# Kernel optimization log

Measured on AMD Instinct MI355X. Metric: run time of the kernel, lower is better.

## Reference

```python
import jax, jax.numpy as jnp
import numpy as np

C_M, C_Z, H, C = 256, 128, 8, 32  # msa emb, pair emb, heads, head channels
S, R = 128, 256                   # MSA rows, residues


def layer_norm(x, gamma, beta, eps=1e-5):
    mu = jnp.mean(x, axis=-1, keepdims=True)
    var = jnp.var(x, axis=-1, keepdims=True)
    return (x - mu) * jax.lax.rsqrt(var + eps) * gamma + beta


def setup_inputs() -> dict:
    key = jax.random.key(0)
    ks = jax.random.split(key, 12)
    sc_m = 1.0 / np.sqrt(C_M)
    sc_z = 1.0 / np.sqrt(C_Z)
    sc_hc = 1.0 / np.sqrt(H * C)
    return {
        "msa_rep": jax.random.normal(ks[0], (S, R, C_M), dtype=jnp.float32),
        "pair_rep": jax.random.normal(ks[1], (R, R, C_Z), dtype=jnp.float32),
        "ln_msa_g": jnp.ones((C_M,), jnp.float32),
        "ln_msa_b": jnp.zeros((C_M,), jnp.float32),
        "ln_pair_g": jnp.ones((C_Z,), jnp.float32),
        "ln_pair_b": jnp.zeros((C_Z,), jnp.float32),
        "w_q": jax.random.normal(ks[2], (C_M, H, C), jnp.float32) * sc_m,
        "w_k": jax.random.normal(ks[3], (C_M, H, C), jnp.float32) * sc_m,
        "w_v": jax.random.normal(ks[4], (C_M, H, C), jnp.float32) * sc_m,
        "w_g": jax.random.normal(ks[5], (C_M, H, C), jnp.float32) * sc_m,
        "b_g": jnp.zeros((H, C), jnp.float32),
        "w_b": jax.random.normal(ks[6], (C_Z, H), jnp.float32) * sc_z,
        "b_b": jnp.zeros((H,), jnp.float32),
        "w_o": jax.random.normal(ks[7], (H, C, C_M), jnp.float32) * sc_hc,
        "b_o": jnp.zeros((C_M,), jnp.float32),
    }


def reference(msa_rep, pair_rep, ln_msa_g, ln_msa_b, ln_pair_g, ln_pair_b,
              w_q, w_k, w_v, w_g, b_g, w_b, b_b, w_o, b_o):
    m = layer_norm(msa_rep, ln_msa_g, ln_msa_b)                 # [S,R,C_M]
    q = jnp.einsum('src,chd->srhd', m, w_q)                     # [S,R,H,C]
    k = jnp.einsum('src,chd->srhd', m, w_k)
    v = jnp.einsum('src,chd->srhd', m, w_v)
    gates = jax.nn.sigmoid(jnp.einsum('src,chd->srhd', m, w_g) + b_g)
    # pair bias: [R,R,H] -> [H,R,R]
    z = layer_norm(pair_rep, ln_pair_g, ln_pair_b)
    b = jnp.einsum('ijc,ch->hij', z, w_b) + b_b[:, None, None]  # [H,R,R]
    logits = jnp.einsum('sqhd,skhd->shqk', q, k) / np.sqrt(C)   # [S,H,R,R]
    logits = logits + b[None]
    w = jax.nn.softmax(logits, axis=-1)
    o = jnp.einsum('shqk,skhd->sqhd', w, v)                     # [S,R,H,C]
    o = gates * o
    out = jnp.einsum('srhd,hdc->src', o, w_o) + b_o             # [S,R,C_M]
    return out
```

## Files before the change

kernel.cpp:

```cpp
#include <hip/hip_runtime.h>
#include <hip/hip_bf16.h>

#define S_DIM 128
#define R_DIM 256
#define CM 256
#define CZ 128
#define H_DIM 8
#define C_DIM 32

typedef short bf16x8 __attribute__((ext_vector_type(8)));
typedef float f32x4 __attribute__((ext_vector_type(4)));

__device__ inline ushort f2b(float f) {
  __hip_bfloat16 b = __float2bfloat16(f);
  return *(ushort*)&b;
}
__device__ inline float b2f(ushort u) {
  __hip_bfloat16 b = *(__hip_bfloat16*)&u;
  return __bfloat162float(b);
}

__device__ __forceinline__ void gld_lds16(const ushort* g, ushort* l) {
  __builtin_amdgcn_global_load_lds(
      (const __attribute__((address_space(1))) unsigned int*)g,
      (__attribute__((address_space(3))) unsigned int*)l, 16, 0, 0);
}

__global__ __launch_bounds__(256) void wt_kernel(
    const float* __restrict__ wq, const float* __restrict__ wk,
    const float* __restrict__ wv, const float* __restrict__ wg,
    const float* __restrict__ wo, ushort* __restrict__ Wt5) {
  __shared__ float t[64][65];
  int z = blockIdx.z;
  const float* W = (z == 0) ? wq : (z == 1) ? wk : (z == 2) ? wv
                   : (z == 3) ? wg : wo;
  ushort* Wt = Wt5 + (size_t)z * 65536;
  int tid = threadIdx.x;
  int r = tid >> 2, c4 = (tid & 3) * 16;
  int rowBase = blockIdx.y * 64, colBase = blockIdx.x * 64;
#pragma unroll
  for (int j = 0; j < 16; ++j)
    t[r][c4 + j] = W[(size_t)(rowBase + r) * 256 + colBase + c4 + j];
  __syncthreads();
#pragma unroll
  for (int j = 0; j < 16; ++j)
    Wt[(size_t)(colBase + r) * 256 + rowBase + c4 + j] = f2b(t[c4 + j][r]);
}

__global__ __launch_bounds__(256) void ln_msa_kernel(
    const float* __restrict__ x, const float* __restrict__ g,
    const float* __restrict__ b, ushort* __restrict__ m) {
  int lane = threadIdx.x & 63, w = threadIdx.x >> 6;
  int row = blockIdx.x * 4 + w;
  const float* xp = x + (size_t)row * CM + lane * 4;
  float4 v = *(const float4*)xp;
  float s1 = v.x + v.y + v.z + v.w;
  float s2 = v.x * v.x + v.y * v.y + v.z * v.z + v.w * v.w;
#pragma unroll
  for (int off = 32; off; off >>= 1) {
    s1 += __shfl_xor(s1, off, 64);
    s2 += __shfl_xor(s2, off, 64);
  }
  float mean = s1 * (1.0f / CM);
  float rstd = rsqrtf(s2 * (1.0f / CM) - mean * mean + 1e-5f);
  float4 gv = *(const float4*)(g + lane * 4);
  float4 bv = *(const float4*)(b + lane * 4);
  ushort4 o;
  o.x = f2b((v.x - mean) * rstd * gv.x + bv.x);
  o.y = f2b((v.y - mean) * rstd * gv.y + bv.y);
  o.z = f2b((v.z - mean) * rstd * gv.z + bv.z);
  o.w = f2b((v.w - mean) * rstd * gv.w + bv.w);
  *(ushort4*)(m + (size_t)row * CM + lane * 4) = o;
}

__global__ __launch_bounds__(256) void pair_bias_kernel(
    const float* __restrict__ z, const float* __restrict__ g,
    const float* __restrict__ b, const float* __restrict__ w_b,
    const float* __restrict__ b_b, float* __restrict__ bias) {
  __shared__ float wbs[CZ][8];
  __shared__ float gs[CZ], bs[CZ];
  int tid = threadIdx.x;
  if (tid < CZ) { gs[tid] = g[tid]; bs[tid] = b[tid]; }
  for (int i = tid; i < CZ * 8; i += 256) wbs[i >> 3][i & 7] = w_b[i];
  __syncthreads();
  int q = tid & 3;
  int row = blockIdx.x * 64 + (tid >> 2);
  const float* zp = z + (size_t)row * CZ + q * 32;
  float4 v[8];
#pragma unroll
  for (int j = 0; j < 8; ++j) v[j] = *(const float4*)(zp + j * 4);
  float s1 = 0.f, s2 = 0.f;
#pragma unroll
  for (int j = 0; j < 8; ++j) {
    s1 += v[j].x + v[j].y + v[j].z + v[j].w;
    s2 += v[j].x * v[j].x + v[j].y * v[j].y + v[j].z * v[j].z +
          v[j].w * v[j].w;
  }
  s1 += __shfl_xor(s1, 1, 64);
  s2 += __shfl_xor(s2, 1, 64);
  s1 += __shfl_xor(s1, 2, 64);
  s2 += __shfl_xor(s2, 2, 64);
  float mean = s1 * (1.0f / CZ);
  float var = s2 * (1.0f / CZ) - mean * mean;
  float rstd = rsqrtf(var + 1e-5f);
  float acc[8] = {};
#pragma unroll
  for (int j = 0; j < 8; ++j) {
    float e[4] = {v[j].x, v[j].y, v[j].z, v[j].w};
#pragma unroll
    for (int u = 0; u < 4; ++u) {
      int c = q * 32 + j * 4 + u;
      float zn = (e[u] - mean) * rstd * gs[c] + bs[c];
#pragma unroll
      for (int h = 0; h < 8; ++h) acc[h] += zn * wbs[c][h];
    }
  }
#pragma unroll
  for (int h = 0; h < 8; ++h) {
    acc[h] += __shfl_xor(acc[h], 1, 64);
    acc[h] += __shfl_xor(acc[h], 2, 64);
  }
  int h0 = q * 2;
  bias[(size_t)h0 * (R_DIM * R_DIM) + row] = acc[h0] + b_b[h0];
  bias[(size_t)(h0 + 1) * (R_DIM * R_DIM) + row] = acc[h0 + 1] + b_b[h0 + 1];
}

__global__ __launch_bounds__(256) void proj_mfma(
    const ushort* __restrict__ M, const ushort* __restrict__ Wt5,
    const float* __restrict__ b_g, ushort* __restrict__ qb,
    ushort* __restrict__ kb2, ushort* __restrict__ vb,
    ushort* __restrict__ gb) {
  __shared__ ushort As[128 * 64];
  __shared__ ushort Bs[64 * 64];
  int tid = threadIdx.x, lane = tid & 63, wid = tid >> 6;
  int lr = lane & 15, lg = lane >> 4;
  int rowBase = blockIdx.x * 128;
  int cby = blockIdx.y;
  int proj = cby >> 2;
  int sc = (lane & 7) ^ ((lane >> 3) & 7);
  const ushort* Ag =
      M + (size_t)(rowBase + wid * 32 + (lane >> 3)) * 256 + sc * 8;
  const ushort* Bg =
      Wt5 + (size_t)(cby * 64 + wid * 16 + (lane >> 3)) * 256 + sc * 8;
  ushort* Asl = As + wid * (32 * 64);
  ushort* Bsl = Bs + wid * (16 * 64);
  int wr = wid >> 1, wc = wid & 1;
  int sx = (lr & 7) * 8;
  f32x4 zf = {0.f, 0.f, 0.f, 0.f};
  f32x4 acc[4][2];
#pragma unroll
  for (int i = 0; i < 4; ++i)
#pragma unroll
    for (int j = 0; j < 2; ++j) acc[i][j] = zf;

  for (int kb = 0; kb < 4; ++kb) {
    if (kb) __syncthreads();
#pragma unroll
    for (int c = 0; c < 4; ++c)
      gld_lds16(Ag + kb * 64 + c * (8 * 256), Asl + c * (8 * 64));
#pragma unroll
    for (int c = 0; c < 2; ++c)
      gld_lds16(Bg + kb * 64 + c * (8 * 256), Bsl + c * (8 * 64));
    __syncthreads();
#pragma unroll
    for (int kk = 0; kk < 2; ++kk) {
      bf16x8 a[4], b[2];
#pragma unroll
      for (int mf = 0; mf < 4; ++mf)
        a[mf] = *(const bf16x8*)&As[(wr * 64 + mf * 16 + lr) * 64 +
                                    ((kk * 32 + lg * 8) ^ sx)];
#pragma unroll
      for (int nf = 0; nf < 2; ++nf)
        b[nf] = *(const bf16x8*)&Bs[(wc * 32 + nf * 16 + lr) * 64 +
                                    ((kk * 32 + lg * 8) ^ sx)];
#pragma unroll
      for (int mf = 0; mf < 4; ++mf)
#pragma unroll
        for (int nf = 0; nf < 2; ++nf)
          acc[mf][nf] = __builtin_amdgcn_mfma_f32_16x16x32_bf16(
              b[nf], a[mf], acc[mf][nf], 0, 0, 0);
    }
  }
#pragma unroll
  for (int mf = 0; mf < 4; ++mf) {
    int row = rowBase + wr * 64 + mf * 16 + lr;
    int s = row >> 8, rr = row & 255;
#pragma unroll
    for (int nf = 0; nf < 2; ++nf) {
      int colL = (cby & 3) * 64 + wc * 32 + nf * 16 + lg * 4;
      int h = colL >> 5, d0 = colL & 31;
      size_t oidx = ((size_t)((s * H_DIM + h) * R_DIM + rr)) * C_DIM + d0;
      f32x4 v4 = acc[mf][nf];
      ushort4 o4;
      if (proj == 0) {
        o4.x = f2b(v4[0] * 0.17677669529663687f);
        o4.y = f2b(v4[1] * 0.17677669529663687f);
        o4.z = f2b(v4[2] * 0.17677669529663687f);
        o4.w = f2b(v4[3] * 0.17677669529663687f);
        *(ushort4*)(qb + oidx) = o4;
      } else if (proj == 1) {
        o4.x = f2b(v4[0]); o4.y = f2b(v4[1]);
        o4.z = f2b(v4[2]); o4.w = f2b(v4[3]);
        *(ushort4*)(kb2 + oidx) = o4;
      } else if (proj == 2) {
        o4.x = f2b(v4[0]); o4.y = f2b(v4[1]);
        o4.z = f2b(v4[2]); o4.w = f2b(v4[3]);
        *(ushort4*)(vb + oidx) = o4;
      } else {
        float4 bg4 = *(const float4*)(b_g + colL);
        o4.x = f2b(1.f / (1.f + __expf(-(v4[0] + bg4.x))));
        o4.y = f2b(1.f / (1.f + __expf(-(v4[1] + bg4.y))));
        o4.z = f2b(1.f / (1.f + __expf(-(v4[2] + bg4.z))));
        o4.w = f2b(1.f / (1.f + __expf(-(v4[3] + bg4.w))));
        *(ushort4*)(gb + oidx) = o4;
      }
    }
  }
}

__global__ __launch_bounds__(512, 4) void attn_mfma(
    const ushort* __restrict__ q, const ushort* __restrict__ k,
    const ushort* __restrict__ v, const ushort* __restrict__ g,
    const float* __restrict__ bias, ushort* __restrict__ ob) {
  __shared__ ushort Vt[32][264];
  __shared__ ushort Pl[8][32][72];
  int blk = blockIdx.x;
  int s = blk >> 3, h = blk & 7;
  int tid = threadIdx.x, lane = tid & 63, w = tid >> 6;
  int lr = lane & 15, lg = lane >> 4;
  size_t base = (size_t)(s * H_DIM + h) * (R_DIM * C_DIM);

  {
    int key = tid >> 1, half = (tid & 1) * 16;
    const ushort* vp = v + base + (size_t)key * 32 + half;
    bf16x8 t0 = *(const bf16x8*)vp;
    bf16x8 t1 = *(const bf16x8*)(vp + 8);
#pragma unroll
    for (int j = 0; j < 8; ++j) {
      Vt[half + j][key] = (ushort)t0[j];
      Vt[half + 8 + j][key] = (ushort)t1[j];
    }
  }
  __syncthreads();

  int qrow0 = w * 32;
  bf16x8 qf[2];
#pragma unroll
  for (int mf = 0; mf < 2; ++mf)
    qf[mf] = *(const bf16x8*)(q + base + (size_t)(qrow0 + mf * 16 + lr) * 32 +
                              lg * 8);
  const float* bp0 = bias + ((size_t)h * R_DIM + qrow0 + lg * 4) * R_DIM +
                     lr * 4;

  float lsum[2][4] = {};
  f32x4 of[2][2];
  f32x4 zf = {0.f, 0.f, 0.f, 0.f};
#pragma unroll
  for (int mf = 0; mf < 2; ++mf) {
    of[mf][0] = zf;
    of[mf][1] = zf;
  }

  bf16x8 kf[4];
#pragma unroll
  for (int nf = 0; nf < 4; ++nf)
    kf[nf] = *(const bf16x8*)(k + base + (size_t)(lr * 4 + nf) * 32 + lg * 8);

#pragma unroll
  for (int t = 0; t < 4; ++t) {
    int k0 = t * 64;
    bf16x8 kfn[4];
    if (t < 3) {
#pragma unroll
      for (int nf = 0; nf < 4; ++nf)
        kfn[nf] = *(const bf16x8*)(k + base +
                                   (size_t)(k0 + 64 + lr * 4 + nf) * 32 +
                                   lg * 8);
    }
    f32x4 sf[2][4];
    __builtin_amdgcn_s_setprio(1);
#pragma unroll
    for (int mf = 0; mf < 2; ++mf)
#pragma unroll
      for (int nf = 0; nf < 4; ++nf)
        sf[mf][nf] =
            __builtin_amdgcn_mfma_f32_16x16x32_bf16(qf[mf], kf[nf], zf, 0, 0, 0);
    __builtin_amdgcn_s_setprio(0);
#pragma unroll
    for (int mf = 0; mf < 2; ++mf) {
      float4 bv[4];
#pragma unroll
      for (int r = 0; r < 4; ++r)
        bv[r] = *(const float4*)(bp0 + (size_t)(mf * 16 + r) * R_DIM + k0);
#pragma unroll
      for (int r = 0; r < 4; ++r) {
        float p0 = __expf(sf[mf][0][r] + bv[r].x);
        float p1 = __expf(sf[mf][1][r] + bv[r].y);
        float p2 = __expf(sf[mf][2][r] + bv[r].z);
        float p3 = __expf(sf[mf][3][r] + bv[r].w);
        lsum[mf][r] += (p0 + p1) + (p2 + p3);
        ushort4 pk;
        pk.x = f2b(p0);
        pk.y = f2b(p1);
        pk.z = f2b(p2);
        pk.w = f2b(p3);
        *(ushort4*)&Pl[w][mf * 16 + lg * 4 + r][lr * 4] = pk;
      }
    }
    __builtin_amdgcn_s_setprio(1);
#pragma unroll
    for (int kt = 0; kt < 2; ++kt) {
      bf16x8 pf[2], vf[2];
#pragma unroll
      for (int mf = 0; mf < 2; ++mf)
        pf[mf] = *(const bf16x8*)&Pl[w][mf * 16 + lr][kt * 32 + lg * 8];
#pragma unroll
      for (int df = 0; df < 2; ++df)
        vf[df] = *(const bf16x8*)&Vt[df * 16 + lr][k0 + kt * 32 + lg * 8];
#pragma unroll
      for (int mf = 0; mf < 2; ++mf)
#pragma unroll
        for (int df = 0; df < 2; ++df)
          of[mf][df] = __builtin_amdgcn_mfma_f32_16x16x32_bf16(
              vf[df], pf[mf], of[mf][df], 0, 0, 0);
    }
    __builtin_amdgcn_s_setprio(0);
    if (t < 3) {
#pragma unroll
      for (int nf = 0; nf < 4; ++nf) kf[nf] = kfn[nf];
    }
  }
#pragma unroll
  for (int mf = 0; mf < 2; ++mf)
#pragma unroll
    for (int r = 0; r < 4; ++r) {
#pragma unroll
      for (int msk = 1; msk <= 8; msk <<= 1)
        lsum[mf][r] += __shfl_xor(lsum[mf][r], msk, 64);
    }
  int srcl = ((lr >> 2) << 4) + lr;
  float invr[2];
#pragma unroll
  for (int mf = 0; mf < 2; ++mf) {
    float t0 = __shfl(lsum[mf][0], srcl, 64);
    float t1 = __shfl(lsum[mf][1], srcl, 64);
    float t2 = __shfl(lsum[mf][2], srcl, 64);
    float t3 = __shfl(lsum[mf][3], srcl, 64);
    int rb = lr & 3;
    float lv = rb == 0 ? t0 : rb == 1 ? t1 : rb == 2 ? t2 : t3;
    invr[mf] = 1.f / lv;
  }
#pragma unroll
  for (int mf = 0; mf < 2; ++mf) {
    int row = qrow0 + mf * 16 + lr;
#pragma unroll
    for (int df = 0; df < 2; ++df) {
      int d0 = df * 16 + lg * 4;
      ushort4 g4 = *(const ushort4*)(g + base + (size_t)row * 32 + d0);
      ushort4 o4;
      o4.x = f2b(of[mf][df][0] * invr[mf] * b2f(g4.x));
      o4.y = f2b(of[mf][df][1] * invr[mf] * b2f(g4.y));
      o4.z = f2b(of[mf][df][2] * invr[mf] * b2f(g4.z));
      o4.w = f2b(of[mf][df][3] * invr[mf] * b2f(g4.w));
      *(ushort4*)(ob + ((size_t)(s * R_DIM + row)) * 256 + h * 32 + d0) = o4;
    }
  }
}

__global__ __launch_bounds__(256) void out_mfma(
    const ushort* __restrict__ A, const ushort* __restrict__ Wt,
    const float* __restrict__ b_o, float* __restrict__ out) {
  __shared__ ushort As[128 * 64];
  __shared__ ushort Bs[64 * 64];
  int tid = threadIdx.x, lane = tid & 63, wid = tid >> 6;
  int lr = lane & 15, lg = lane >> 4;
  int rowBase = blockIdx.x * 128;
  int colBase = blockIdx.y * 64;
  int sc = (lane & 7) ^ ((lane >> 3) & 7);
  const ushort* Ag =
      A + (size_t)(rowBase + wid * 32 + (lane >> 3)) * 256 + sc * 8;
  const ushort* Bg =
      Wt + (size_t)(colBase + wid * 16 + (lane >> 3)) * 256 + sc * 8;
  ushort* Asl = As + wid * (32 * 64);
  ushort* Bsl = Bs + wid * (16 * 64);
  int wr = wid >> 1, wc = wid & 1;
  int sx = (lr & 7) * 8;
  f32x4 zf = {0.f, 0.f, 0.f, 0.f};
  f32x4 acc[4][2];
#pragma unroll
  for (int i = 0; i < 4; ++i)
#pragma unroll
    for (int j = 0; j < 2; ++j) acc[i][j] = zf;

  for (int kb = 0; kb < 4; ++kb) {
    if (kb) __syncthreads();
#pragma unroll
    for (int c = 0; c < 4; ++c)
      gld_lds16(Ag + kb * 64 + c * (8 * 256), Asl + c * (8 * 64));
#pragma unroll
    for (int c = 0; c < 2; ++c)
      gld_lds16(Bg + kb * 64 + c * (8 * 256), Bsl + c * (8 * 64));
    __syncthreads();
#pragma unroll
    for (int kk = 0; kk < 2; ++kk) {
      bf16x8 a[4], b[2];
#pragma unroll
      for (int mf = 0; mf < 4; ++mf)
        a[mf] = *(const bf16x8*)&As[(wr * 64 + mf * 16 + lr) * 64 +
                                    ((kk * 32 + lg * 8) ^ sx)];
#pragma unroll
      for (int nf = 0; nf < 2; ++nf)
        b[nf] = *(const bf16x8*)&Bs[(wc * 32 + nf * 16 + lr) * 64 +
                                    ((kk * 32 + lg * 8) ^ sx)];
#pragma unroll
      for (int mf = 0; mf < 4; ++mf)
#pragma unroll
        for (int nf = 0; nf < 2; ++nf)
          acc[mf][nf] = __builtin_amdgcn_mfma_f32_16x16x32_bf16(
              b[nf], a[mf], acc[mf][nf], 0, 0, 0);
    }
  }
#pragma unroll
  for (int mf = 0; mf < 4; ++mf) {
    int row = rowBase + wr * 64 + mf * 16 + lr;
#pragma unroll
    for (int nf = 0; nf < 2; ++nf) {
      int col0 = colBase + wc * 32 + nf * 16 + lg * 4;
      float4 bo4 = *(const float4*)(b_o + col0);
      float4 o4;
      o4.x = acc[mf][nf][0] + bo4.x;
      o4.y = acc[mf][nf][1] + bo4.y;
      o4.z = acc[mf][nf][2] + bo4.z;
      o4.w = acc[mf][nf][3] + bo4.w;
      *(float4*)(out + (size_t)row * 256 + col0) = o4;
    }
  }
}

extern "C" void kernel_launch(void* const* d_in, const int* in_sizes, int n_in,
                              void* d_out, int out_size, void* d_ws,
                              size_t ws_size, hipStream_t stream) {
  const float* msa      = (const float*)d_in[0];
  const float* pair     = (const float*)d_in[1];
  const float* ln_msa_g = (const float*)d_in[2];
  const float* ln_msa_b = (const float*)d_in[3];
  const float* ln_pr_g  = (const float*)d_in[4];
  const float* ln_pr_b  = (const float*)d_in[5];
  const float* w_q      = (const float*)d_in[6];
  const float* w_k      = (const float*)d_in[7];
  const float* w_v      = (const float*)d_in[8];
  const float* w_g      = (const float*)d_in[9];
  const float* b_g      = (const float*)d_in[10];
  const float* w_b      = (const float*)d_in[11];
  const float* b_b      = (const float*)d_in[12];
  const float* w_o      = (const float*)d_in[13];
  const float* b_o      = (const float*)d_in[14];
  float* out = (float*)d_out;

  char* ws = (char*)d_ws;
  ushort* m   = (ushort*)(ws + 0);
  ushort* qb  = (ushort*)(ws + 16777216ull);
  ushort* kb  = (ushort*)(ws + 33554432ull);
  ushort* vb  = (ushort*)(ws + 50331648ull);
  ushort* gb  = (ushort*)(ws + 67108864ull);
  float*  bi  = (float*) (ws + 83886080ull);
  ushort* ob  = (ushort*)(ws + 85983232ull);
  ushort* Wt5 = (ushort*)(ws + 102760448ull);

  wt_kernel<<<dim3(4, 4, 5), 256, 0, stream>>>(w_q, w_k, w_v, w_g, w_o, Wt5);
  ln_msa_kernel<<<S_DIM * R_DIM / 4, 256, 0, stream>>>(msa, ln_msa_g,
                                                       ln_msa_b, m);
  pair_bias_kernel<<<R_DIM * R_DIM / 64, 256, 0, stream>>>(
      pair, ln_pr_g, ln_pr_b, w_b, b_b, bi);
  proj_mfma<<<dim3(256, 16), 256, 0, stream>>>(m, Wt5, b_g, qb, kb, vb, gb);
  attn_mfma<<<S_DIM * H_DIM, 512, 0, stream>>>(qb, kb, vb, gb, bi, ob);
  out_mfma<<<dim3(256, 4), 256, 0, stream>>>(ob, Wt5 + 4 * 65536, b_o, out);
}
```

Before: 117.5 us.

## Merge prologue kernels into one launch and widen GEMM column tiles to 128

The three independent prologue kernels (weight transpose, MSA layernorm, pair-bias) are merged into one launch that dispatches on block index ranges. This removes two launch gaps and lets the three jobs run concurrently. The projection and output GEMMs now compute 128 output columns per block instead of 64, so each A tile loaded into LDS is reused twice and the grid is halved. The cost is twice the accumulator registers and more LDS per block, which may lower occupancy.

```diff
diff --git a/kernel.cpp b/kernel.cpp
--- a/kernel.cpp
+++ b/kernel.cpp
@@ -26,103 +26,104 @@
       (__attribute__((address_space(3))) unsigned int*)l, 16, 0, 0);
 }
 
-__global__ __launch_bounds__(256) void wt_kernel(
+__global__ __launch_bounds__(256) void prologue_kernel(
+    const float* __restrict__ msa, const float* __restrict__ ln_msa_g,
+    const float* __restrict__ ln_msa_b, ushort* __restrict__ m,
+    const float* __restrict__ pair, const float* __restrict__ ln_pr_g,
+    const float* __restrict__ ln_pr_b, const float* __restrict__ w_b,
+    const float* __restrict__ b_b, float* __restrict__ bias,
     const float* __restrict__ wq, const float* __restrict__ wk,
     const float* __restrict__ wv, const float* __restrict__ wg,
     const float* __restrict__ wo, ushort* __restrict__ Wt5) {
   __shared__ float t[64][65];
-  int z = blockIdx.z;
-  const float* W = (z == 0) ? wq : (z == 1) ? wk : (z == 2) ? wv
-                   : (z == 3) ? wg : wo;
-  ushort* Wt = Wt5 + (size_t)z * 65536;
-  int tid = threadIdx.x;
-  int r = tid >> 2, c4 = (tid & 3) * 16;
-  int rowBase = blockIdx.y * 64, colBase = blockIdx.x * 64;
-#pragma unroll
-  for (int j = 0; j < 16; ++j)
-    t[r][c4 + j] = W[(size_t)(rowBase + r) * 256 + colBase + c4 + j];
-  __syncthreads();
-#pragma unroll
-  for (int j = 0; j < 16; ++j)
-    Wt[(size_t)(colBase + r) * 256 + rowBase + c4 + j] = f2b(t[c4 + j][r]);
-}
-
-__global__ __launch_bounds__(256) void ln_msa_kernel(
-    const float* __restrict__ x, const float* __restrict__ g,
-    const float* __restrict__ b, ushort* __restrict__ m) {
-  int lane = threadIdx.x & 63, w = threadIdx.x >> 6;
-  int row = blockIdx.x * 4 + w;
-  const float* xp = x + (size_t)row * CM + lane * 4;
-  float4 v = *(const float4*)xp;
-  float s1 = v.x + v.y + v.z + v.w;
-  float s2 = v.x * v.x + v.y * v.y + v.z * v.z + v.w * v.w;
-#pragma unroll
-  for (int off = 32; off; off >>= 1) {
-    s1 += __shfl_xor(s1, off, 64);
-    s2 += __shfl_xor(s2, off, 64);
-  }
-  float mean = s1 * (1.0f / CM);
-  float rstd = rsqrtf(s2 * (1.0f / CM) - mean * mean + 1e-5f);
-  float4 gv = *(const float4*)(g + lane * 4);
-  float4 bv = *(const float4*)(b + lane * 4);
-  ushort4 o;
-  o.x = f2b((v.x - mean) * rstd * gv.x + bv.x);
-  o.y = f2b((v.y - mean) * rstd * gv.y + bv.y);
-  o.z = f2b((v.z - mean) * rstd * gv.z + bv.z);
-  o.w = f2b((v.w - mean) * rstd * gv.w + bv.w);
-  *(ushort4*)(m + (size_t)row * CM + lane * 4) = o;
-}
-
-__global__ __launch_bounds__(256) void pair_bias_kernel(
-    const float* __restrict__ z, const float* __restrict__ g,
-    const float* __restrict__ b, const float* __restrict__ w_b,
-    const float* __restrict__ b_b, float* __restrict__ bias) {
   __shared__ float wbs[CZ][8];
   __shared__ float gs[CZ], bs[CZ];
+  int b = blockIdx.x;
   int tid = threadIdx.x;
-  if (tid < CZ) { gs[tid] = g[tid]; bs[tid] = b[tid]; }
-  for (int i = tid; i < CZ * 8; i += 256) wbs[i >> 3][i & 7] = w_b[i];
-  __syncthreads();
-  int q = tid & 3;
-  int row = blockIdx.x * 64 + (tid >> 2);
-  const float* zp = z + (size_t)row * CZ + q * 32;
-  float4 v[8];
-#pragma unroll
-  for (int j = 0; j < 8; ++j) v[j] = *(const float4*)(zp + j * 4);
-  float s1 = 0.f, s2 = 0.f;
-#pragma unroll
-  for (int j = 0; j < 8; ++j) {
-    s1 += v[j].x + v[j].y + v[j].z + v[j].w;
-    s2 += v[j].x * v[j].x + v[j].y * v[j].y + v[j].z * v[j].z +
-          v[j].w * v[j].w;
-  }
-  s1 += __shfl_xor(s1, 1, 64);
-  s2 += __shfl_xor(s2, 1, 64);
-  s1 += __shfl_xor(s1, 2, 64);
-  s2 += __shfl_xor(s2, 2, 64);
-  float mean = s1 * (1.0f / CZ);
-  float var = s2 * (1.0f / CZ) - mean * mean;
-  float rstd = rsqrtf(var + 1e-5f);
-  float acc[8] = {};
-#pragma unroll
-  for (int j = 0; j < 8; ++j) {
-    float e[4] = {v[j].x, v[j].y, v[j].z, v[j].w};
-#pragma unroll
-    for (int u = 0; u < 4; ++u) {
-      int c = q * 32 + j * 4 + u;
-      float zn = (e[u] - mean) * rstd * gs[c] + bs[c];
-#pragma unroll
-      for (int h = 0; h < 8; ++h) acc[h] += zn * wbs[c][h];
-    }
-  }
-#pragma unroll
-  for (int h = 0; h < 8; ++h) {
-    acc[h] += __shfl_xor(acc[h], 1, 64);
-    acc[h] += __shfl_xor(acc[h], 2, 64);
-  }
-  int h0 = q * 2;
-  bias[(size_t)h0 * (R_DIM * R_DIM) + row] = acc[h0] + b_b[h0];
-  bias[(size_t)(h0 + 1) * (R_DIM * R_DIM) + row] = acc[h0 + 1] + b_b[h0 + 1];
+  if (b < 8192) {
+    int lane = tid & 63, w = tid >> 6;
+    int row = b * 4 + w;
+    const float* xp = msa + (size_t)row * CM + lane * 4;
+    float4 v = *(const float4*)xp;
+    float s1 = v.x + v.y + v.z + v.w;
+    float s2 = v.x * v.x + v.y * v.y + v.z * v.z + v.w * v.w;
+#pragma unroll
+    for (int off = 32; off; off >>= 1) {
+      s1 += __shfl_xor(s1, off, 64);
+      s2 += __shfl_xor(s2, off, 64);
+    }
+    float mean = s1 * (1.0f / CM);
+    float rstd = rsqrtf(s2 * (1.0f / CM) - mean * mean + 1e-5f);
+    float4 gv = *(const float4*)(ln_msa_g + lane * 4);
+    float4 bv = *(const float4*)(ln_msa_b + lane * 4);
+    ushort4 o;
+    o.x = f2b((v.x - mean) * rstd * gv.x + bv.x);
+    o.y = f2b((v.y - mean) * rstd * gv.y + bv.y);
+    o.z = f2b((v.z - mean) * rstd * gv.z + bv.z);
+    o.w = f2b((v.w - mean) * rstd * gv.w + bv.w);
+    *(ushort4*)(m + (size_t)row * CM + lane * 4) = o;
+  } else if (b < 9216) {
+    int bb = b - 8192;
+    if (tid < CZ) { gs[tid] = ln_pr_g[tid]; bs[tid] = ln_pr_b[tid]; }
+    for (int i = tid; i < CZ * 8; i += 256) wbs[i >> 3][i & 7] = w_b[i];
+    __syncthreads();
+    int q = tid & 3;
+    int row = bb * 64 + (tid >> 2);
+    const float* zp = pair + (size_t)row * CZ + q * 32;
+    float4 v[8];
+#pragma unroll
+    for (int j = 0; j < 8; ++j) v[j] = *(const float4*)(zp + j * 4);
+    float s1 = 0.f, s2 = 0.f;
+#pragma unroll
+    for (int j = 0; j < 8; ++j) {
+      s1 += v[j].x + v[j].y + v[j].z + v[j].w;
+      s2 += v[j].x * v[j].x + v[j].y * v[j].y + v[j].z * v[j].z +
+            v[j].w * v[j].w;
+    }
+    s1 += __shfl_xor(s1, 1, 64);
+    s2 += __shfl_xor(s2, 1, 64);
+    s1 += __shfl_xor(s1, 2, 64);
+    s2 += __shfl_xor(s2, 2, 64);
+    float mean = s1 * (1.0f / CZ);
+    float var = s2 * (1.0f / CZ) - mean * mean;
+    float rstd = rsqrtf(var + 1e-5f);
+    float acc[8] = {};
+#pragma unroll
+    for (int j = 0; j < 8; ++j) {
+      float e[4] = {v[j].x, v[j].y, v[j].z, v[j].w};
+#pragma unroll
+      for (int u = 0; u < 4; ++u) {
+        int c = q * 32 + j * 4 + u;
+        float zn = (e[u] - mean) * rstd * gs[c] + bs[c];
+#pragma unroll
+        for (int h = 0; h < 8; ++h) acc[h] += zn * wbs[c][h];
+      }
+    }
+#pragma unroll
+    for (int h = 0; h < 8; ++h) {
+      acc[h] += __shfl_xor(acc[h], 1, 64);
+      acc[h] += __shfl_xor(acc[h], 2, 64);
+    }
+    int h0 = q * 2;
+    bias[(size_t)h0 * (R_DIM * R_DIM) + row] = acc[h0] + b_b[h0];
+    bias[(size_t)(h0 + 1) * (R_DIM * R_DIM) + row] = acc[h0 + 1] + b_b[h0 + 1];
+  } else {
+    int zz = b - 9216;
+    int z = zz >> 4, rem = zz & 15;
+    int by = rem >> 2, bx = rem & 3;
+    const float* W = (z == 0) ? wq : (z == 1) ? wk : (z == 2) ? wv
+                     : (z == 3) ? wg : wo;
+    ushort* Wt = Wt5 + (size_t)z * 65536;
+    int r = tid >> 2, c4 = (tid & 3) * 16;
+    int rowBase = by * 64, colBase = bx * 64;
+#pragma unroll
+    for (int j = 0; j < 16; ++j)
+      t[r][c4 + j] = W[(size_t)(rowBase + r) * 256 + colBase + c4 + j];
+    __syncthreads();
+#pragma unroll
+    for (int j = 0; j < 16; ++j)
+      Wt[(size_t)(colBase + r) * 256 + rowBase + c4 + j] = f2b(t[c4 + j][r]);
+  }
 }
 
 __global__ __launch_bounds__(256) void proj_mfma(
@@ -131,27 +132,31 @@
     ushort* __restrict__ kb2, ushort* __restrict__ vb,
     ushort* __restrict__ gb) {
   __shared__ ushort As[128 * 64];
-  __shared__ ushort Bs[64 * 64];
+  __shared__ ushort Bs[2][64 * 64];
   int tid = threadIdx.x, lane = tid & 63, wid = tid >> 6;
   int lr = lane & 15, lg = lane >> 4;
   int rowBase = blockIdx.x * 128;
   int cby = blockIdx.y;
-  int proj = cby >> 2;
+  int proj = cby >> 1;
   int sc = (lane & 7) ^ ((lane >> 3) & 7);
   const ushort* Ag =
       M + (size_t)(rowBase + wid * 32 + (lane >> 3)) * 256 + sc * 8;
-  const ushort* Bg =
-      Wt5 + (size_t)(cby * 64 + wid * 16 + (lane >> 3)) * 256 + sc * 8;
+  const ushort* Bg0 =
+      Wt5 + (size_t)(cby * 128 + wid * 16 + (lane >> 3)) * 256 + sc * 8;
+  const ushort* Bg1 = Bg0 + (size_t)64 * 256;
   ushort* Asl = As + wid * (32 * 64);
-  ushort* Bsl = Bs + wid * (16 * 64);
+  ushort* Bsl0 = Bs[0] + wid * (16 * 64);
+  ushort* Bsl1 = Bs[1] + wid * (16 * 64);
   int wr = wid >> 1, wc = wid & 1;
   int sx = (lr & 7) * 8;
   f32x4 zf = {0.f, 0.f, 0.f, 0.f};
-  f32x4 acc[4][2];
-#pragma unroll
-  for (int i = 0; i < 4; ++i)
-#pragma unroll
-    for (int j = 0; j < 2; ++j) acc[i][j] = zf;
+  f32x4 acc[2][4][2];
+#pragma unroll
+  for (int c = 0; c < 2; ++c)
+#pragma unroll
+    for (int i = 0; i < 4; ++i)
+#pragma unroll
+      for (int j = 0; j < 2; ++j) acc[c][i][j] = zf;
 
   for (int kb = 0; kb < 4; ++kb) {
     if (kb) __syncthreads();
@@ -159,63 +164,73 @@
     for (int c = 0; c < 4; ++c)
       gld_lds16(Ag + kb * 64 + c * (8 * 256), Asl + c * (8 * 64));
 #pragma unroll
-    for (int c = 0; c < 2; ++c)
-      gld_lds16(Bg + kb * 64 + c * (8 * 256), Bsl + c * (8 * 64));
+    for (int c = 0; c < 2; ++c) {
+      gld_lds16(Bg0 + kb * 64 + c * (8 * 256), Bsl0 + c * (8 * 64));
+      gld_lds16(Bg1 + kb * 64 + c * (8 * 256), Bsl1 + c * (8 * 64));
+    }
     __syncthreads();
 #pragma unroll
     for (int kk = 0; kk < 2; ++kk) {
-      bf16x8 a[4], b[2];
+      bf16x8 a[4], b0[2], b1[2];
 #pragma unroll
       for (int mf = 0; mf < 4; ++mf)
         a[mf] = *(const bf16x8*)&As[(wr * 64 + mf * 16 + lr) * 64 +
                                     ((kk * 32 + lg * 8) ^ sx)];
 #pragma unroll
-      for (int nf = 0; nf < 2; ++nf)
-        b[nf] = *(const bf16x8*)&Bs[(wc * 32 + nf * 16 + lr) * 64 +
-                                    ((kk * 32 + lg * 8) ^ sx)];
+      for (int nf = 0; nf < 2; ++nf) {
+        b0[nf] = *(const bf16x8*)&Bs[0][(wc * 32 + nf * 16 + lr) * 64 +
+                                        ((kk * 32 + lg * 8) ^ sx)];
+        b1[nf] = *(const bf16x8*)&Bs[1][(wc * 32 + nf * 16 + lr) * 64 +
+                                        ((kk * 32 + lg * 8) ^ sx)];
+      }
 #pragma unroll
       for (int mf = 0; mf < 4; ++mf)
 #pragma unroll
-        for (int nf = 0; nf < 2; ++nf)
-          acc[mf][nf] = __builtin_amdgcn_mfma_f32_16x16x32_bf16(
-              b[nf], a[mf], acc[mf][nf], 0, 0, 0);
-    }
-  }
-#pragma unroll
-  for (int mf = 0; mf < 4; ++mf) {
-    int row = rowBase + wr * 64 + mf * 16 + lr;
-    int s = row >> 8, rr = row & 255;
-#pragma unroll
-    for (int nf = 0; nf < 2; ++nf) {
-      int colL = (cby & 3) * 64 + wc * 32 + nf * 16 + lg * 4;
-      int h = colL >> 5, d0 = colL & 31;
-      size_t oidx = ((size_t)((s * H_DIM + h) * R_DIM + rr)) * C_DIM + d0;
-      f32x4 v4 = acc[mf][nf];
-      ushort4 o4;
-      if (proj == 0) {
-        o4.x = f2b(v4[0] * 0.17677669529663687f);
-        o4.y = f2b(v4[1] * 0.17677669529663687f);
-        o4.z = f2b(v4[2] * 0.17677669529663687f);
-        o4.w = f2b(v4[3] * 0.17677669529663687f);
-        *(ushort4*)(qb + oidx) = o4;
-      } else if (proj == 1) {
-        o4.x = f2b(v4[0]); o4.y = f2b(v4[1]);
-        o4.z = f2b(v4[2]); o4.w = f2b(v4[3]);
-        *(ushort4*)(kb2 + oidx) = o4;
-      } else if (proj == 2) {
-        o4.x = f2b(v4[0]); o4.y = f2b(v4[1]);
-        o4.z = f2b(v4[2]); o4.w = f2b(v4[3]);
-        *(ushort4*)(vb + oidx) = o4;
-      } else {
-        float4 bg4 = *(const float4*)(b_g + colL);
-        o4.x = f2b(1.f / (1.f + __expf(-(v4[0] + bg4.x))));
-        o4.y = f2b(1.f / (1.f + __expf(-(v4[1] + bg4.y))));
-        o4.z = f2b(1.f / (1.f + __expf(-(v4[2] + bg4.z))));
-        o4.w = f2b(1.f / (1.f + __expf(-(v4[3] + bg4.w))));
-        *(ushort4*)(gb + oidx) = o4;
+        for (int nf = 0; nf < 2; ++nf) {
+          acc[0][mf][nf] = __builtin_amdgcn_mfma_f32_16x16x32_bf16(
+              b0[nf], a[mf], acc[0][mf][nf], 0, 0, 0);
+          acc[1][mf][nf] = __builtin_amdgcn_mfma_f32_16x16x32_bf16(
+              b1[nf], a[mf], acc[1][mf][nf], 0, 0, 0);
+        }
+    }
+  }
+#pragma unroll
+  for (int cc = 0; cc < 2; ++cc)
+#pragma unroll
+    for (int mf = 0; mf < 4; ++mf) {
+      int row = rowBase + wr * 64 + mf * 16 + lr;
+      int s = row >> 8, rr = row & 255;
+#pragma unroll
+      for (int nf = 0; nf < 2; ++nf) {
+        int colL = (cby & 1) * 128 + cc * 64 + wc * 32 + nf * 16 + lg * 4;
+        int h = colL >> 5, d0 = colL & 31;
+        size_t oidx = ((size_t)((s * H_DIM + h) * R_DIM + rr)) * C_DIM + d0;
+        f32x4 v4 = acc[cc][mf][nf];
+        ushort4 o4;
+        if (proj == 0) {
+          o4.x = f2b(v4[0] * 0.17677669529663687f);
+          o4.y = f2b(v4[1] * 0.17677669529663687f);
+          o4.z = f2b(v4[2] * 0.17677669529663687f);
+          o4.w = f2b(v4[3] * 0.17677669529663687f);
+          *(ushort4*)(qb + oidx) = o4;
+        } else if (proj == 1) {
+          o4.x = f2b(v4[0]); o4.y = f2b(v4[1]);
+          o4.z = f2b(v4[2]); o4.w = f2b(v4[3]);
+          *(ushort4*)(kb2 + oidx) = o4;
+        } else if (proj == 2) {
+          o4.x = f2b(v4[0]); o4.y = f2b(v4[1]);
+          o4.z = f2b(v4[2]); o4.w = f2b(v4[3]);
+          *(ushort4*)(vb + oidx) = o4;
+        } else {
+          float4 bg4 = *(const float4*)(b_g + colL);
+          o4.x = f2b(1.f / (1.f + __expf(-(v4[0] + bg4.x))));
+          o4.y = f2b(1.f / (1.f + __expf(-(v4[1] + bg4.y))));
+          o4.z = f2b(1.f / (1.f + __expf(-(v4[2] + bg4.z))));
+          o4.w = f2b(1.f / (1.f + __expf(-(v4[3] + bg4.w))));
+          *(ushort4*)(gb + oidx) = o4;
+        }
       }
     }
-  }
 }
 
 __global__ __launch_bounds__(512, 4) void attn_mfma(
@@ -371,26 +386,30 @@
     const ushort* __restrict__ A, const ushort* __restrict__ Wt,
     const float* __restrict__ b_o, float* __restrict__ out) {
   __shared__ ushort As[128 * 64];
-  __shared__ ushort Bs[64 * 64];
+  __shared__ ushort Bs[2][64 * 64];
   int tid = threadIdx.x, lane = tid & 63, wid = tid >> 6;
   int lr = lane & 15, lg = lane >> 4;
   int rowBase = blockIdx.x * 128;
-  int colBase = blockIdx.y * 64;
+  int cby = blockIdx.y;
   int sc = (lane & 7) ^ ((lane >> 3) & 7);
   const ushort* Ag =
       A + (size_t)(rowBase + wid * 32 + (lane >> 3)) * 256 + sc * 8;
-  const ushort* Bg =
-      Wt + (size_t)(colBase + wid * 16 + (lane >> 3)) * 256 + sc * 8;
+  const ushort* Bg0 =
+      Wt + (size_t)(cby * 128 + wid * 16 + (lane >> 3)) * 256 + sc * 8;
+  const ushort* Bg1 = Bg0 + (size_t)64 * 256;
   ushort* Asl = As + wid * (32 * 64);
-  ushort* Bsl = Bs + wid * (16 * 64);
+  ushort* Bsl0 = Bs[0] + wid * (16 * 64);
+  ushort* Bsl1 = Bs[1] + wid * (16 * 64);
   int wr = wid >> 1, wc = wid & 1;
   int sx = (lr & 7) * 8;
   f32x4 zf = {0.f, 0.f, 0.f, 0.f};
-  f32x4 acc[4][2];
-#pragma unroll
-  for (int i = 0; i < 4; ++i)
-#pragma unroll
-    for (int j = 0; j < 2; ++j) acc[i][j] = zf;
+  f32x4 acc[2][4][2];
+#pragma unroll
+  for (int c = 0; c < 2; ++c)
+#pragma unroll
+    for (int i = 0; i < 4; ++i)
+#pragma unroll
+      for (int j = 0; j < 2; ++j) acc[c][i][j] = zf;
 
   for (int kb = 0; kb < 4; ++kb) {
     if (kb) __syncthreads();
@@ -398,43 +417,53 @@
     for (int c = 0; c < 4; ++c)
       gld_lds16(Ag + kb * 64 + c * (8 * 256), Asl + c * (8 * 64));
 #pragma unroll
-    for (int c = 0; c < 2; ++c)
-      gld_lds16(Bg + kb * 64 + c * (8 * 256), Bsl + c * (8 * 64));
+    for (int c = 0; c < 2; ++c) {
+      gld_lds16(Bg0 + kb * 64 + c * (8 * 256), Bsl0 + c * (8 * 64));
+      gld_lds16(Bg1 + kb * 64 + c * (8 * 256), Bsl1 + c * (8 * 64));
+    }
     __syncthreads();
 #pragma unroll
     for (int kk = 0; kk < 2; ++kk) {
-      bf16x8 a[4], b[2];
+      bf16x8 a[4], b0[2], b1[2];
 #pragma unroll
       for (int mf = 0; mf < 4; ++mf)
         a[mf] = *(const bf16x8*)&As[(wr * 64 + mf * 16 + lr) * 64 +
                                     ((kk * 32 + lg * 8) ^ sx)];
 #pragma unroll
-      for (int nf = 0; nf < 2; ++nf)
-        b[nf] = *(const bf16x8*)&Bs[(wc * 32 + nf * 16 + lr) * 64 +
-                                    ((kk * 32 + lg * 8) ^ sx)];
+      for (int nf = 0; nf < 2; ++nf) {
+        b0[nf] = *(const bf16x8*)&Bs[0][(wc * 32 + nf * 16 + lr) * 64 +
+                                        ((kk * 32 + lg * 8) ^ sx)];
+        b1[nf] = *(const bf16x8*)&Bs[1][(wc * 32 + nf * 16 + lr) * 64 +
+                                        ((kk * 32 + lg * 8) ^ sx)];
+      }
 #pragma unroll
       for (int mf = 0; mf < 4; ++mf)
 #pragma unroll
-        for (int nf = 0; nf < 2; ++nf)
-          acc[mf][nf] = __builtin_amdgcn_mfma_f32_16x16x32_bf16(
-              b[nf], a[mf], acc[mf][nf], 0, 0, 0);
-    }
-  }
-#pragma unroll
-  for (int mf = 0; mf < 4; ++mf) {
-    int row = rowBase + wr * 64 + mf * 16 + lr;
-#pragma unroll
-    for (int nf = 0; nf < 2; ++nf) {
-      int col0 = colBase + wc * 32 + nf * 16 + lg * 4;
-      float4 bo4 = *(const float4*)(b_o + col0);
-      float4 o4;
-      o4.x = acc[mf][nf][0] + bo4.x;
-      o4.y = acc[mf][nf][1] + bo4.y;
-      o4.z = acc[mf][nf][2] + bo4.z;
-      o4.w = acc[mf][nf][3] + bo4.w;
-      *(float4*)(out + (size_t)row * 256 + col0) = o4;
-    }
-  }
+        for (int nf = 0; nf < 2; ++nf) {
+          acc[0][mf][nf] = __builtin_amdgcn_mfma_f32_16x16x32_bf16(
+              b0[nf], a[mf], acc[0][mf][nf], 0, 0, 0);
+          acc[1][mf][nf] = __builtin_amdgcn_mfma_f32_16x16x32_bf16(
+              b1[nf], a[mf], acc[1][mf][nf], 0, 0, 0);
+        }
+    }
+  }
+#pragma unroll
+  for (int cc = 0; cc < 2; ++cc)
+#pragma unroll
+    for (int mf = 0; mf < 4; ++mf) {
+      int row = rowBase + wr * 64 + mf * 16 + lr;
+#pragma unroll
+      for (int nf = 0; nf < 2; ++nf) {
+        int col0 = cby * 128 + cc * 64 + wc * 32 + nf * 16 + lg * 4;
+        float4 bo4 = *(const float4*)(b_o + col0);
+        float4 o4;
+        o4.x = acc[cc][mf][nf][0] + bo4.x;
+        o4.y = acc[cc][mf][nf][1] + bo4.y;
+        o4.z = acc[cc][mf][nf][2] + bo4.z;
+        o4.w = acc[cc][mf][nf][3] + bo4.w;
+        *(float4*)(out + (size_t)row * 256 + col0) = o4;
+      }
+    }
 }
 
 extern "C" void kernel_launch(void* const* d_in, const int* in_sizes, int n_in,
@@ -467,12 +496,10 @@
   ushort* ob  = (ushort*)(ws + 85983232ull);
   ushort* Wt5 = (ushort*)(ws + 102760448ull);
 
-  wt_kernel<<<dim3(4, 4, 5), 256, 0, stream>>>(w_q, w_k, w_v, w_g, w_o, Wt5);
-  ln_msa_kernel<<<S_DIM * R_DIM / 4, 256, 0, stream>>>(msa, ln_msa_g,
-                                                       ln_msa_b, m);
-  pair_bias_kernel<<<R_DIM * R_DIM / 64, 256, 0, stream>>>(
-      pair, ln_pr_g, ln_pr_b, w_b, b_b, bi);
-  proj_mfma<<<dim3(256, 16), 256, 0, stream>>>(m, Wt5, b_g, qb, kb, vb, gb);
+  prologue_kernel<<<9296, 256, 0, stream>>>(
+      msa, ln_msa_g, ln_msa_b, m, pair, ln_pr_g, ln_pr_b, w_b, b_b, bi,
+      w_q, w_k, w_v, w_g, w_o, Wt5);
+  proj_mfma<<<dim3(256, 8), 256, 0, stream>>>(m, Wt5, b_g, qb, kb, vb, gb);
   attn_mfma<<<S_DIM * H_DIM, 512, 0, stream>>>(qb, kb, vb, gb, bi, ob);
-  out_mfma<<<dim3(256, 4), 256, 0, stream>>>(ob, Wt5 + 4 * 65536, b_o, out);
-}
+  out_mfma<<<dim3(256, 2), 256, 0, stream>>>(ob, Wt5 + 4 * 65536, b_o, out);
+}
```

After: 113.0 us, median of 2. 1.04x faster.

## Merge prologue kernels and double-buffer LDS loads in projection GEMMs

Applied to the files above, without the earlier changes.

Folds the weight-transpose, MSA layernorm and pair-bias kernels into one launch that branches on block index, removing two kernel launches and their gaps. The projection and output GEMMs now keep two LDS buffers and issue the next K-tile's global-to-LDS loads before computing the current one, using explicit vmcnt waits and barriers. This doubles LDS use per block, which may lower occupancy, and the prologue's shared-memory footprint becomes the union of all three branches.

```diff
diff --git a/kernel.cpp b/kernel.cpp
--- a/kernel.cpp
+++ b/kernel.cpp
@@ -26,103 +26,104 @@
       (__attribute__((address_space(3))) unsigned int*)l, 16, 0, 0);
 }
 
-__global__ __launch_bounds__(256) void wt_kernel(
+__global__ __launch_bounds__(256) void prologue_kernel(
+    const float* __restrict__ msa, const float* __restrict__ ln_msa_g,
+    const float* __restrict__ ln_msa_b, ushort* __restrict__ m,
+    const float* __restrict__ pair, const float* __restrict__ ln_pr_g,
+    const float* __restrict__ ln_pr_b, const float* __restrict__ w_b,
+    const float* __restrict__ b_b, float* __restrict__ bias,
     const float* __restrict__ wq, const float* __restrict__ wk,
     const float* __restrict__ wv, const float* __restrict__ wg,
     const float* __restrict__ wo, ushort* __restrict__ Wt5) {
   __shared__ float t[64][65];
-  int z = blockIdx.z;
-  const float* W = (z == 0) ? wq : (z == 1) ? wk : (z == 2) ? wv
-                   : (z == 3) ? wg : wo;
-  ushort* Wt = Wt5 + (size_t)z * 65536;
-  int tid = threadIdx.x;
-  int r = tid >> 2, c4 = (tid & 3) * 16;
-  int rowBase = blockIdx.y * 64, colBase = blockIdx.x * 64;
-#pragma unroll
-  for (int j = 0; j < 16; ++j)
-    t[r][c4 + j] = W[(size_t)(rowBase + r) * 256 + colBase + c4 + j];
-  __syncthreads();
-#pragma unroll
-  for (int j = 0; j < 16; ++j)
-    Wt[(size_t)(colBase + r) * 256 + rowBase + c4 + j] = f2b(t[c4 + j][r]);
-}
-
-__global__ __launch_bounds__(256) void ln_msa_kernel(
-    const float* __restrict__ x, const float* __restrict__ g,
-    const float* __restrict__ b, ushort* __restrict__ m) {
-  int lane = threadIdx.x & 63, w = threadIdx.x >> 6;
-  int row = blockIdx.x * 4 + w;
-  const float* xp = x + (size_t)row * CM + lane * 4;
-  float4 v = *(const float4*)xp;
-  float s1 = v.x + v.y + v.z + v.w;
-  float s2 = v.x * v.x + v.y * v.y + v.z * v.z + v.w * v.w;
-#pragma unroll
-  for (int off = 32; off; off >>= 1) {
-    s1 += __shfl_xor(s1, off, 64);
-    s2 += __shfl_xor(s2, off, 64);
-  }
-  float mean = s1 * (1.0f / CM);
-  float rstd = rsqrtf(s2 * (1.0f / CM) - mean * mean + 1e-5f);
-  float4 gv = *(const float4*)(g + lane * 4);
-  float4 bv = *(const float4*)(b + lane * 4);
-  ushort4 o;
-  o.x = f2b((v.x - mean) * rstd * gv.x + bv.x);
-  o.y = f2b((v.y - mean) * rstd * gv.y + bv.y);
-  o.z = f2b((v.z - mean) * rstd * gv.z + bv.z);
-  o.w = f2b((v.w - mean) * rstd * gv.w + bv.w);
-  *(ushort4*)(m + (size_t)row * CM + lane * 4) = o;
-}
-
-__global__ __launch_bounds__(256) void pair_bias_kernel(
-    const float* __restrict__ z, const float* __restrict__ g,
-    const float* __restrict__ b, const float* __restrict__ w_b,
-    const float* __restrict__ b_b, float* __restrict__ bias) {
   __shared__ float wbs[CZ][8];
   __shared__ float gs[CZ], bs[CZ];
+  int b = blockIdx.x;
   int tid = threadIdx.x;
-  if (tid < CZ) { gs[tid] = g[tid]; bs[tid] = b[tid]; }
-  for (int i = tid; i < CZ * 8; i += 256) wbs[i >> 3][i & 7] = w_b[i];
-  __syncthreads();
-  int q = tid & 3;
-  int row = blockIdx.x * 64 + (tid >> 2);
-  const float* zp = z + (size_t)row * CZ + q * 32;
-  float4 v[8];
-#pragma unroll
-  for (int j = 0; j < 8; ++j) v[j] = *(const float4*)(zp + j * 4);
-  float s1 = 0.f, s2 = 0.f;
-#pragma unroll
-  for (int j = 0; j < 8; ++j) {
-    s1 += v[j].x + v[j].y + v[j].z + v[j].w;
-    s2 += v[j].x * v[j].x + v[j].y * v[j].y + v[j].z * v[j].z +
-          v[j].w * v[j].w;
-  }
-  s1 += __shfl_xor(s1, 1, 64);
-  s2 += __shfl_xor(s2, 1, 64);
-  s1 += __shfl_xor(s1, 2, 64);
-  s2 += __shfl_xor(s2, 2, 64);
-  float mean = s1 * (1.0f / CZ);
-  float var = s2 * (1.0f / CZ) - mean * mean;
-  float rstd = rsqrtf(var + 1e-5f);
-  float acc[8] = {};
-#pragma unroll
-  for (int j = 0; j < 8; ++j) {
-    float e[4] = {v[j].x, v[j].y, v[j].z, v[j].w};
-#pragma unroll
-    for (int u = 0; u < 4; ++u) {
-      int c = q * 32 + j * 4 + u;
-      float zn = (e[u] - mean) * rstd * gs[c] + bs[c];
-#pragma unroll
-      for (int h = 0; h < 8; ++h) acc[h] += zn * wbs[c][h];
-    }
-  }
-#pragma unroll
-  for (int h = 0; h < 8; ++h) {
-    acc[h] += __shfl_xor(acc[h], 1, 64);
-    acc[h] += __shfl_xor(acc[h], 2, 64);
-  }
-  int h0 = q * 2;
-  bias[(size_t)h0 * (R_DIM * R_DIM) + row] = acc[h0] + b_b[h0];
-  bias[(size_t)(h0 + 1) * (R_DIM * R_DIM) + row] = acc[h0 + 1] + b_b[h0 + 1];
+  if (b < 8192) {
+    int lane = tid & 63, w = tid >> 6;
+    int row = b * 4 + w;
+    const float* xp = msa + (size_t)row * CM + lane * 4;
+    float4 v = *(const float4*)xp;
+    float s1 = v.x + v.y + v.z + v.w;
+    float s2 = v.x * v.x + v.y * v.y + v.z * v.z + v.w * v.w;
+#pragma unroll
+    for (int off = 32; off; off >>= 1) {
+      s1 += __shfl_xor(s1, off, 64);
+      s2 += __shfl_xor(s2, off, 64);
+    }
+    float mean = s1 * (1.0f / CM);
+    float rstd = rsqrtf(s2 * (1.0f / CM) - mean * mean + 1e-5f);
+    float4 gv = *(const float4*)(ln_msa_g + lane * 4);
+    float4 bv = *(const float4*)(ln_msa_b + lane * 4);
+    ushort4 o;
+    o.x = f2b((v.x - mean) * rstd * gv.x + bv.x);
+    o.y = f2b((v.y - mean) * rstd * gv.y + bv.y);
+    o.z = f2b((v.z - mean) * rstd * gv.z + bv.z);
+    o.w = f2b((v.w - mean) * rstd * gv.w + bv.w);
+    *(ushort4*)(m + (size_t)row * CM + lane * 4) = o;
+  } else if (b < 9216) {
+    int bb = b - 8192;
+    if (tid < CZ) { gs[tid] = ln_pr_g[tid]; bs[tid] = ln_pr_b[tid]; }
+    for (int i = tid; i < CZ * 8; i += 256) wbs[i >> 3][i & 7] = w_b[i];
+    __syncthreads();
+    int q = tid & 3;
+    int row = bb * 64 + (tid >> 2);
+    const float* zp = pair + (size_t)row * CZ + q * 32;
+    float4 v[8];
+#pragma unroll
+    for (int j = 0; j < 8; ++j) v[j] = *(const float4*)(zp + j * 4);
+    float s1 = 0.f, s2 = 0.f;
+#pragma unroll
+    for (int j = 0; j < 8; ++j) {
+      s1 += v[j].x + v[j].y + v[j].z + v[j].w;
+      s2 += v[j].x * v[j].x + v[j].y * v[j].y + v[j].z * v[j].z +
+            v[j].w * v[j].w;
+    }
+    s1 += __shfl_xor(s1, 1, 64);
+    s2 += __shfl_xor(s2, 1, 64);
+    s1 += __shfl_xor(s1, 2, 64);
+    s2 += __shfl_xor(s2, 2, 64);
+    float mean = s1 * (1.0f / CZ);
+    float var = s2 * (1.0f / CZ) - mean * mean;
+    float rstd = rsqrtf(var + 1e-5f);
+    float acc[8] = {};
+#pragma unroll
+    for (int j = 0; j < 8; ++j) {
+      float e[4] = {v[j].x, v[j].y, v[j].z, v[j].w};
+#pragma unroll
+      for (int u = 0; u < 4; ++u) {
+        int c = q * 32 + j * 4 + u;
+        float zn = (e[u] - mean) * rstd * gs[c] + bs[c];
+#pragma unroll
+        for (int h = 0; h < 8; ++h) acc[h] += zn * wbs[c][h];
+      }
+    }
+#pragma unroll
+    for (int h = 0; h < 8; ++h) {
+      acc[h] += __shfl_xor(acc[h], 1, 64);
+      acc[h] += __shfl_xor(acc[h], 2, 64);
+    }
+    int h0 = q * 2;
+    bias[(size_t)h0 * (R_DIM * R_DIM) + row] = acc[h0] + b_b[h0];
+    bias[(size_t)(h0 + 1) * (R_DIM * R_DIM) + row] = acc[h0 + 1] + b_b[h0 + 1];
+  } else {
+    int zz = b - 9216;
+    int z = zz >> 4, rem = zz & 15;
+    int by = rem >> 2, bx = rem & 3;
+    const float* W = (z == 0) ? wq : (z == 1) ? wk : (z == 2) ? wv
+                     : (z == 3) ? wg : wo;
+    ushort* Wt = Wt5 + (size_t)z * 65536;
+    int r = tid >> 2, c4 = (tid & 3) * 16;
+    int rowBase = by * 64, colBase = bx * 64;
+#pragma unroll
+    for (int j = 0; j < 16; ++j)
+      t[r][c4 + j] = W[(size_t)(rowBase + r) * 256 + colBase + c4 + j];
+    __syncthreads();
+#pragma unroll
+    for (int j = 0; j < 16; ++j)
+      Wt[(size_t)(colBase + r) * 256 + rowBase + c4 + j] = f2b(t[c4 + j][r]);
+  }
 }
 
 __global__ __launch_bounds__(256) void proj_mfma(
@@ -130,8 +131,8 @@
     const float* __restrict__ b_g, ushort* __restrict__ qb,
     ushort* __restrict__ kb2, ushort* __restrict__ vb,
     ushort* __restrict__ gb) {
-  __shared__ ushort As[128 * 64];
-  __shared__ ushort Bs[64 * 64];
+  __shared__ ushort As[2][128 * 64];
+  __shared__ ushort Bs[2][64 * 64];
   int tid = threadIdx.x, lane = tid & 63, wid = tid >> 6;
   int lr = lane & 15, lg = lane >> 4;
   int rowBase = blockIdx.x * 128;
@@ -142,8 +143,8 @@
       M + (size_t)(rowBase + wid * 32 + (lane >> 3)) * 256 + sc * 8;
   const ushort* Bg =
       Wt5 + (size_t)(cby * 64 + wid * 16 + (lane >> 3)) * 256 + sc * 8;
-  ushort* Asl = As + wid * (32 * 64);
-  ushort* Bsl = Bs + wid * (16 * 64);
+  int aoff = wid * (32 * 64);
+  int boff = wid * (16 * 64);
   int wr = wid >> 1, wc = wid & 1;
   int sx = (lr & 7) * 8;
   f32x4 zf = {0.f, 0.f, 0.f, 0.f};
@@ -153,26 +154,43 @@
 #pragma unroll
     for (int j = 0; j < 2; ++j) acc[i][j] = zf;
 
+#pragma unroll
+  for (int c = 0; c < 4; ++c)
+    gld_lds16(Ag + c * (8 * 256), &As[0][aoff + c * (8 * 64)]);
+#pragma unroll
+  for (int c = 0; c < 2; ++c)
+    gld_lds16(Bg + c * (8 * 256), &Bs[0][boff + c * (8 * 64)]);
+
+#pragma unroll
   for (int kb = 0; kb < 4; ++kb) {
-    if (kb) __syncthreads();
-#pragma unroll
-    for (int c = 0; c < 4; ++c)
-      gld_lds16(Ag + kb * 64 + c * (8 * 256), Asl + c * (8 * 64));
-#pragma unroll
-    for (int c = 0; c < 2; ++c)
-      gld_lds16(Bg + kb * 64 + c * (8 * 256), Bsl + c * (8 * 64));
-    __syncthreads();
+    const int cur = kb & 1;
+    if (kb < 3) {
+#pragma unroll
+      for (int c = 0; c < 4; ++c)
+        gld_lds16(Ag + (kb + 1) * 64 + c * (8 * 256),
+                  &As[cur ^ 1][aoff + c * (8 * 64)]);
+#pragma unroll
+      for (int c = 0; c < 2; ++c)
+        gld_lds16(Bg + (kb + 1) * 64 + c * (8 * 256),
+                  &Bs[cur ^ 1][boff + c * (8 * 64)]);
+      asm volatile("s_waitcnt vmcnt(6)" ::: "memory");
+    } else {
+      asm volatile("s_waitcnt vmcnt(0)" ::: "memory");
+    }
+    __builtin_amdgcn_sched_barrier(0);
+    __builtin_amdgcn_s_barrier();
+    __builtin_amdgcn_sched_barrier(0);
 #pragma unroll
     for (int kk = 0; kk < 2; ++kk) {
       bf16x8 a[4], b[2];
 #pragma unroll
       for (int mf = 0; mf < 4; ++mf)
-        a[mf] = *(const bf16x8*)&As[(wr * 64 + mf * 16 + lr) * 64 +
-                                    ((kk * 32 + lg * 8) ^ sx)];
+        a[mf] = *(const bf16x8*)&As[cur][(wr * 64 + mf * 16 + lr) * 64 +
+                                         ((kk * 32 + lg * 8) ^ sx)];
 #pragma unroll
       for (int nf = 0; nf < 2; ++nf)
-        b[nf] = *(const bf16x8*)&Bs[(wc * 32 + nf * 16 + lr) * 64 +
-                                    ((kk * 32 + lg * 8) ^ sx)];
+        b[nf] = *(const bf16x8*)&Bs[cur][(wc * 32 + nf * 16 + lr) * 64 +
+                                         ((kk * 32 + lg * 8) ^ sx)];
 #pragma unroll
       for (int mf = 0; mf < 4; ++mf)
 #pragma unroll
@@ -180,6 +198,9 @@
           acc[mf][nf] = __builtin_amdgcn_mfma_f32_16x16x32_bf16(
               b[nf], a[mf], acc[mf][nf], 0, 0, 0);
     }
+    __builtin_amdgcn_sched_barrier(0);
+    __builtin_amdgcn_s_barrier();
+    __builtin_amdgcn_sched_barrier(0);
   }
 #pragma unroll
   for (int mf = 0; mf < 4; ++mf) {
@@ -370,8 +391,8 @@
 __global__ __launch_bounds__(256) void out_mfma(
     const ushort* __restrict__ A, const ushort* __restrict__ Wt,
     const float* __restrict__ b_o, float* __restrict__ out) {
-  __shared__ ushort As[128 * 64];
-  __shared__ ushort Bs[64 * 64];
+  __shared__ ushort As[2][128 * 64];
+  __shared__ ushort Bs[2][64 * 64];
   int tid = threadIdx.x, lane = tid & 63, wid = tid >> 6;
   int lr = lane & 15, lg = lane >> 4;
   int rowBase = blockIdx.x * 128;
@@ -381,8 +402,8 @@
       A + (size_t)(rowBase + wid * 32 + (lane >> 3)) * 256 + sc * 8;
   const ushort* Bg =
       Wt + (size_t)(colBase + wid * 16 + (lane >> 3)) * 256 + sc * 8;
-  ushort* Asl = As + wid * (32 * 64);
-  ushort* Bsl = Bs + wid * (16 * 64);
+  int aoff = wid * (32 * 64);
+  int boff = wid * (16 * 64);
   int wr = wid >> 1, wc = wid & 1;
   int sx = (lr & 7) * 8;
   f32x4 zf = {0.f, 0.f, 0.f, 0.f};
@@ -392,26 +413,43 @@
 #pragma unroll
     for (int j = 0; j < 2; ++j) acc[i][j] = zf;
 
+#pragma unroll
+  for (int c = 0; c < 4; ++c)
+    gld_lds16(Ag + c * (8 * 256), &As[0][aoff + c * (8 * 64)]);
+#pragma unroll
+  for (int c = 0; c < 2; ++c)
+    gld_lds16(Bg + c * (8 * 256), &Bs[0][boff + c * (8 * 64)]);
+
+#pragma unroll
   for (int kb = 0; kb < 4; ++kb) {
-    if (kb) __syncthreads();
-#pragma unroll
-    for (int c = 0; c < 4; ++c)
-      gld_lds16(Ag + kb * 64 + c * (8 * 256), Asl + c * (8 * 64));
-#pragma unroll
-    for (int c = 0; c < 2; ++c)
-      gld_lds16(Bg + kb * 64 + c * (8 * 256), Bsl + c * (8 * 64));
-    __syncthreads();
+    const int cur = kb & 1;
+    if (kb < 3) {
+#pragma unroll
+      for (int c = 0; c < 4; ++c)
+        gld_lds16(Ag + (kb + 1) * 64 + c * (8 * 256),
+                  &As[cur ^ 1][aoff + c * (8 * 64)]);
+#pragma unroll
+      for (int c = 0; c < 2; ++c)
+        gld_lds16(Bg + (kb + 1) * 64 + c * (8 * 256),
+                  &Bs[cur ^ 1][boff + c * (8 * 64)]);
+      asm volatile("s_waitcnt vmcnt(6)" ::: "memory");
+    } else {
+      asm volatile("s_waitcnt vmcnt(0)" ::: "memory");
+    }
+    __builtin_amdgcn_sched_barrier(0);
+    __builtin_amdgcn_s_barrier();
+    __builtin_amdgcn_sched_barrier(0);
 #pragma unroll
     for (int kk = 0; kk < 2; ++kk) {
       bf16x8 a[4], b[2];
 #pragma unroll
       for (int mf = 0; mf < 4; ++mf)
-        a[mf] = *(const bf16x8*)&As[(wr * 64 + mf * 16 + lr) * 64 +
-                                    ((kk * 32 + lg * 8) ^ sx)];
+        a[mf] = *(const bf16x8*)&As[cur][(wr * 64 + mf * 16 + lr) * 64 +
+                                         ((kk * 32 + lg * 8) ^ sx)];
 #pragma unroll
       for (int nf = 0; nf < 2; ++nf)
-        b[nf] = *(const bf16x8*)&Bs[(wc * 32 + nf * 16 + lr) * 64 +
-                                    ((kk * 32 + lg * 8) ^ sx)];
+        b[nf] = *(const bf16x8*)&Bs[cur][(wc * 32 + nf * 16 + lr) * 64 +
+                                         ((kk * 32 + lg * 8) ^ sx)];
 #pragma unroll
       for (int mf = 0; mf < 4; ++mf)
 #pragma unroll
@@ -419,6 +457,9 @@
           acc[mf][nf] = __builtin_amdgcn_mfma_f32_16x16x32_bf16(
               b[nf], a[mf], acc[mf][nf], 0, 0, 0);
     }
+    __builtin_amdgcn_sched_barrier(0);
+    __builtin_amdgcn_s_barrier();
+    __builtin_amdgcn_sched_barrier(0);
   }
 #pragma unroll
   for (int mf = 0; mf < 4; ++mf) {
@@ -467,11 +508,9 @@
   ushort* ob  = (ushort*)(ws + 85983232ull);
   ushort* Wt5 = (ushort*)(ws + 102760448ull);
 
-  wt_kernel<<<dim3(4, 4, 5), 256, 0, stream>>>(w_q, w_k, w_v, w_g, w_o, Wt5);
-  ln_msa_kernel<<<S_DIM * R_DIM / 4, 256, 0, stream>>>(msa, ln_msa_g,
-                                                       ln_msa_b, m);
-  pair_bias_kernel<<<R_DIM * R_DIM / 64, 256, 0, stream>>>(
-      pair, ln_pr_g, ln_pr_b, w_b, b_b, bi);
+  prologue_kernel<<<9296, 256, 0, stream>>>(
+      msa, ln_msa_g, ln_msa_b, m, pair, ln_pr_g, ln_pr_b, w_b, b_b, bi,
+      w_q, w_k, w_v, w_g, w_o, Wt5);
   proj_mfma<<<dim3(256, 16), 256, 0, stream>>>(m, Wt5, b_g, qb, kb, vb, gb);
   attn_mfma<<<S_DIM * H_DIM, 512, 0, stream>>>(qb, kb, vb, gb, bi, ob);
   out_mfma<<<dim3(256, 4), 256, 0, stream>>>(ob, Wt5 + 4 * 65536, b_o, out);
```

After: 119.7 us. About the same (+1.8%).
